# Performance work log

Measured on AMD Instinct MI355X. Metric: run time of the kernel, lower is better.

The kernel has to match this reference:

```python
import jax, jax.numpy as jnp
import numpy as np


def setup_inputs() -> dict:
    key = jax.random.key(0)
    k1, k2, k3, k4, k5 = jax.random.split(key, 5)
    B, L, H = 32, 2048, 768
    in1 = jax.random.normal(k1, (B, H), dtype=jnp.float32)
    in2 = jax.random.normal(k2, (B, H), dtype=jnp.float32)
    text = jax.random.normal(k3, (B, L, H), dtype=jnp.float32)
    textmask = jnp.ones((B, L), dtype=jnp.float32)  # 1 = valid token
    # learned params (nn.Linear weights are [out, in]); small scale avoids tanh saturation
    W2 = jax.random.normal(k4, (H, 3 * H), dtype=jnp.float32) * 0.02
    b2 = jnp.zeros((H,), dtype=jnp.float32)
    W1 = jax.random.normal(k5, (1, H), dtype=jnp.float32) * 0.02
    b1 = jnp.zeros((1,), dtype=jnp.float32)
    return {"in1": in1, "in2": in2, "text": text, "textmask": textmask,
            "W2": W2, "b2": b2, "W1": W1, "b1": b1}


def reference(in1, in2, text, textmask, W2, b2, W1, b1):
    H = in1.shape[-1]
    # Split linear2 weight along input dim instead of materializing cat([in1,in2,text]).
    # Same math: cat @ W2.T == in1@W2a.T + in2@W2b.T + text@W2c.T
    W2a, W2b, W2c = W2[:, :H], W2[:, H:2 * H], W2[:, 2 * H:]
    bias_bh = in1 @ W2a.T + in2 @ W2b.T + b2          # [B, H], broadcast over L
    h = jnp.tanh(jnp.einsum('blh,gh->blg', text, W2c) + bias_bh[:, None, :])  # [B, L, H]
    att = jnp.einsum('blh,h->bl', h, W1[0]) + b1[0]   # [B, L]
    att = jax.nn.softmax((1.0 - textmask) * (-1e20) + att, axis=-1)  # masked softmax [B, L]
    context = jnp.einsum('bl,blh->bh', att, text)     # weighted sum [B, H]
    return context, att[:, None, :]                   # matches (context, att[B,1,L])
```

## Files before the change

kernel.cpp:

```cpp
#include <hip/hip_runtime.h>
#include <hip/hip_bf16.h>

typedef __bf16 bf16x8 __attribute__((ext_vector_type(8)));
typedef __bf16 bf16x4 __attribute__((ext_vector_type(4)));
typedef float  f32x4  __attribute__((ext_vector_type(4)));

#define H 768
#define LSEQ 2048
#define BATCH 32
#define MROWS (BATCH*LSEQ)
#define NT 3
#define W2S 2304

__device__ __forceinline__ void gload_lds16(const void* g, void* l){
  __builtin_amdgcn_global_load_lds((const __attribute__((address_space(1))) void*)g,
                                   (__attribute__((address_space(3))) void*)l, 16, 0, 0);
}

__global__ void w2c_cvt_k(const float* __restrict__ W2, __bf16* __restrict__ w2cb){
  int i4 = blockIdx.x*256 + threadIdx.x;
  int g  = i4 / 192;
  int hc = (i4 % 192) * 4;
  f32x4 v = *(const f32x4*)(W2 + (size_t)g*W2S + 1536 + hc);
  bf16x4 o; o[0]=(__bf16)v[0]; o[1]=(__bf16)v[1]; o[2]=(__bf16)v[2]; o[3]=(__bf16)v[3];
  *(bf16x4*)(w2cb + (size_t)g*H + hc) = o;
}

__global__ void bias_k(const float* __restrict__ in1, const float* __restrict__ in2,
                       const float* __restrict__ W2, const float* __restrict__ b2,
                       float* __restrict__ bias){
  int b = blockIdx.y;
  int g = blockIdx.x*64 + (threadIdx.x & 63);
  int q = threadIdx.x >> 6;
  const float* wa = W2 + (size_t)g*W2S + q*192;
  const float* wb = wa + H;
  const float* x1 = in1 + b*H + q*192;
  const float* x2 = in2 + b*H + q*192;
  float acc = 0.f;
  #pragma unroll 8
  for (int h=0; h<192; h+=4){
    f32x4 a4 = *(const f32x4*)(wa+h);
    f32x4 c4 = *(const f32x4*)(x1+h);
    f32x4 b4 = *(const f32x4*)(wb+h);
    f32x4 d4 = *(const f32x4*)(x2+h);
    acc += a4[0]*c4[0]+a4[1]*c4[1]+a4[2]*c4[2]+a4[3]*c4[3];
    acc += b4[0]*d4[0]+b4[1]*d4[1]+b4[2]*d4[2]+b4[3]*d4[3];
  }
  __shared__ float sm[4][64];
  sm[q][threadIdx.x&63] = acc;
  __syncthreads();
  if (q==0){
    float r = sm[0][threadIdx.x]+sm[1][threadIdx.x]+sm[2][threadIdx.x]+sm[3][threadIdx.x] + b2[g];
    bias[(size_t)b*H + g] = r;
  }
}

__global__ __launch_bounds__(256,2) void fused_gemm_att_k(
    const float* __restrict__ text, const __bf16* __restrict__ w2cb,
    const float* __restrict__ bias, const float* __restrict__ W1,
    float* __restrict__ attp)
{
  __shared__ __align__(16) __bf16 a_lds[2][128*32];
  __shared__ __align__(16) __bf16 b_lds[2][256*32];
  __shared__ float att_lds[2][128];

  int bid = blockIdx.x;
  int lin = (bid & 7)*192 + (bid >> 3);
  int mt  = lin / 3;
  int nt  = lin % 3;
  int b   = mt >> 4;
  int m0  = mt << 7;
  int t = threadIdx.x, lane = t & 63, wid = t >> 6;
  int wm = wid >> 1, wn = wid & 1;

  const float*  atile = text + (size_t)m0*H;
  const __bf16* btile = w2cb + (size_t)(nt*256)*H;

  f32x4 acc[4][8];
  #pragma unroll
  for (int mi=0;mi<4;++mi)
    #pragma unroll
    for (int ni=0;ni<8;++ni) acc[mi][ni] = (f32x4){0.f,0.f,0.f,0.f};

  int ar = t>>3, ac = (t&7)*4;
  int ag = (t&7)>>1, ah = t&1;
  f32x4 aReg[4];

  auto loadA = [&](int kk){
    #pragma unroll
    for (int j=0;j<4;++j)
      aReg[j] = *(const f32x4*)(atile + (size_t)(ar + j*32)*H + kk*32 + ac);
  };
  auto writeA = [&](int bf){
    #pragma unroll
    for (int j=0;j<4;++j){
      int row = ar + j*32;
      int gc  = ag ^ ((row>>1)&3);
      bf16x4 o; o[0]=(__bf16)aReg[j][0]; o[1]=(__bf16)aReg[j][1];
                o[2]=(__bf16)aReg[j][2]; o[3]=(__bf16)aReg[j][3];
      *(bf16x4*)&a_lds[bf][row*32 + gc*8 + ah*4] = o;
    }
  };
  auto stageB = [&](int bf, int kk){
    #pragma unroll
    for (int j=0;j<4;++j){
      int slot = wid*4 + j;
      int n  = slot*16 + (lane>>2);
      int gs = (lane&3) ^ ((lane>>3)&3);
      gload_lds16(btile + (size_t)n*H + kk*32 + gs*8, &b_lds[bf][slot*512]);
    }
  };
  auto compute = [&](int bf){
    bf16x8 af[4];
    #pragma unroll
    for (int mi=0;mi<4;++mi){
      int row = wm*64 + mi*16 + (lane&15);
      int rc  = (lane>>4) ^ ((row>>1)&3);
      af[mi] = *(const bf16x8*)&a_lds[bf][row*32 + rc*8];
    }
    #pragma unroll
    for (int ni=0;ni<8;++ni){
      int n  = wn*128 + ni*16 + (lane&15);
      int rc = (lane>>4) ^ ((n>>1)&3);
      bf16x8 bq = *(const bf16x8*)&b_lds[bf][n*32 + rc*8];
      #pragma unroll
      for (int mi=0;mi<4;++mi)
        acc[mi][ni] = __builtin_amdgcn_mfma_f32_16x16x32_bf16(af[mi], bq, acc[mi][ni], 0,0,0);
    }
  };

  loadA(0);
  writeA(0);
  stageB(0, 0);
  loadA(1);
  __syncthreads();

  #pragma unroll 2
  for (int kk=0; kk<22; ++kk){
    int cur = kk&1, nxt = cur^1;
    stageB(nxt, kk+1);
    writeA(nxt);
    loadA(kk+2);
    compute(cur);
    asm volatile("s_waitcnt vmcnt(4) lgkmcnt(0)" ::: "memory");
    __builtin_amdgcn_sched_barrier(0);
    __builtin_amdgcn_s_barrier();
    __builtin_amdgcn_sched_barrier(0);
  }
  {
    stageB(1, 23);
    writeA(1);
    compute(0);
    asm volatile("s_waitcnt vmcnt(0) lgkmcnt(0)" ::: "memory");
    __builtin_amdgcn_sched_barrier(0);
    __builtin_amdgcn_s_barrier();
    __builtin_amdgcn_sched_barrier(0);
  }
  compute(1);

  float bb[8], ww[8];
  int gb = nt*256 + wn*128 + (lane&15);
  #pragma unroll
  for (int ni=0;ni<8;++ni){ bb[ni]=bias[(size_t)b*H + gb + ni*16]; ww[ni]=W1[gb + ni*16]; }

  float av[16];
  #pragma unroll
  for (int mi=0;mi<4;++mi)
    #pragma unroll
    for (int r=0;r<4;++r){
      float s = 0.f;
      #pragma unroll
      for (int ni=0;ni<8;++ni){
        float x = acc[mi][ni][r] + bb[ni];
        float e = __expf(2.0f*x);
        s += ww[ni] * ((e-1.0f)*__builtin_amdgcn_rcpf(e+1.0f));
      }
      av[mi*4+r] = s;
    }
  #pragma unroll
  for (int off=1; off<16; off<<=1)
    #pragma unroll
    for (int i=0;i<16;++i) av[i] += __shfl_xor(av[i], off);

  if ((lane&15)==0){
    int mg = (lane>>4)*4;
    #pragma unroll
    for (int mi=0;mi<4;++mi)
      #pragma unroll
      for (int r=0;r<4;++r)
        att_lds[wn][wm*64 + mi*16 + mg + r] = av[mi*4+r];
  }
  __syncthreads();
  if (t < 128) attp[(size_t)nt*MROWS + m0 + t] = att_lds[0][t] + att_lds[1][t];
}

__global__ void softmax_k(const float* __restrict__ attp, const float* __restrict__ tmask,
                          const float* __restrict__ b1, float* __restrict__ att){
  int b = blockIdx.x, t = threadIdx.x;
  int lane = t & 63, wv = t >> 6;
  __shared__ float sl[LSEQ];
  __shared__ float red[4];
  float b1v = b1[0];
  float lmax = -3.0e38f;
  for (int i=t; i<LSEQ; i+=256){
    float v = b1v;
    #pragma unroll
    for (int p=0;p<NT;++p) v += attp[(size_t)p*MROWS + b*LSEQ + i];
    v += (1.0f - tmask[b*LSEQ+i]) * -1.0e20f;
    sl[i] = v;
    lmax = fmaxf(lmax, v);
  }
  #pragma unroll
  for (int off=32; off>=1; off>>=1) lmax = fmaxf(lmax, __shfl_xor(lmax, off));
  if (lane==0) red[wv] = lmax;
  __syncthreads();
  float mx = fmaxf(fmaxf(red[0],red[1]), fmaxf(red[2],red[3]));
  __syncthreads();
  float lsum = 0.f;
  for (int i=t; i<LSEQ; i+=256){
    float e = __expf(sl[i]-mx);
    sl[i] = e;
    lsum += e;
  }
  #pragma unroll
  for (int off=32; off>=1; off>>=1) lsum += __shfl_xor(lsum, off);
  if (lane==0) red[wv] = lsum;
  __syncthreads();
  float inv = 1.0f/(red[0]+red[1]+red[2]+red[3]);
  for (int i=t; i<LSEQ; i+=256) att[(size_t)b*LSEQ+i] = sl[i]*inv;
}

__global__ void ctxpart_k(const float* __restrict__ text, const float* __restrict__ att,
                          float* __restrict__ ctxp){
  int chunk = blockIdx.x, b = blockIdx.y, t = threadIdx.x;
  const float* tp = text + ((size_t)(b*LSEQ + chunk*64))*H + 4*t;
  const float* ap = att + (size_t)b*LSEQ + chunk*64;
  f32x4 acc = {0.f,0.f,0.f,0.f};
  #pragma unroll 4
  for (int l=0;l<64;++l){
    float a = ap[l];
    f32x4 v = *(const f32x4*)(tp + (size_t)l*H);
    acc[0] += a*v[0]; acc[1] += a*v[1]; acc[2] += a*v[2]; acc[3] += a*v[3];
  }
  *(f32x4*)(ctxp + ((size_t)(b*32+chunk))*H + 4*t) = acc;
}

__global__ void ctxred_k(const float* __restrict__ ctxp, float* __restrict__ out){
  int b = blockIdx.x, h = threadIdx.x;
  float s = 0.f;
  #pragma unroll 8
  for (int c=0;c<32;++c) s += ctxp[((size_t)(b*32+c))*H + h];
  out[(size_t)b*H + h] = s;
}

extern "C" void kernel_launch(void* const* d_in, const int* in_sizes, int n_in,
                              void* d_out, int out_size, void* d_ws, size_t ws_size,
                              hipStream_t stream){
  (void)in_sizes; (void)n_in; (void)out_size; (void)ws_size;
  const float* in1   = (const float*)d_in[0];
  const float* in2   = (const float*)d_in[1];
  const float* text  = (const float*)d_in[2];
  const float* tmask = (const float*)d_in[3];
  const float* W2    = (const float*)d_in[4];
  const float* b2    = (const float*)d_in[5];
  const float* W1    = (const float*)d_in[6];
  const float* b1    = (const float*)d_in[7];
  float* out = (float*)d_out;
  char*  ws  = (char*)d_ws;
  __bf16* w2cb = (__bf16*)(ws);
  float* biasb = (float*)(ws + 1179648);
  float* attp  = (float*)(ws + 1277952);
  float* ctxp  = (float*)(ws + 2850816);
  float* att_out = out + BATCH*H;

  w2c_cvt_k      <<<dim3(576),   dim3(256), 0, stream>>>(W2, w2cb);
  bias_k         <<<dim3(12,32), dim3(256), 0, stream>>>(in1, in2, W2, b2, biasb);
  fused_gemm_att_k<<<dim3(1536), dim3(256), 0, stream>>>(text, w2cb, biasb, W1, attp);
  softmax_k      <<<dim3(32),    dim3(256), 0, stream>>>(attp, tmask, b1, att_out);
  ctxpart_k      <<<dim3(32,32), dim3(192), 0, stream>>>(text, att_out, ctxp);
  ctxred_k       <<<dim3(32),    dim3(768), 0, stream>>>(ctxp, out);
}
```

Before: 182.0 us.

## Retile fused GEMM to 128x128 output tiles with 64-wide K steps

Shrinks each block's N tile from 256 to 128 columns and doubles the K step from 32 to 64, doubling the grid and producing six partial attention sums instead of three. The A-tile load becomes contiguous per thread with wider 16-byte LDS writes, and the XOR swizzles are precomputed. The aim is fewer accumulator registers, better latency hiding and fewer loop iterations and barriers. The cost is that each fp32 text tile is read and converted to bf16 twice as often, and the extra reads must be absorbed by L2.

```diff
diff --git a/kernel.cpp b/kernel.cpp
--- a/kernel.cpp
+++ b/kernel.cpp
@@ -9,7 +9,7 @@
 #define LSEQ 2048
 #define BATCH 32
 #define MROWS (BATCH*LSEQ)
-#define NT 3
+#define NT 6
 #define W2S 2304
 
 __device__ __forceinline__ void gload_lds16(const void* g, void* l){
@@ -60,72 +60,91 @@
     const float* __restrict__ bias, const float* __restrict__ W1,
     float* __restrict__ attp)
 {
-  __shared__ __align__(16) __bf16 a_lds[2][128*32];
-  __shared__ __align__(16) __bf16 b_lds[2][256*32];
+  __shared__ __align__(16) __bf16 a_lds[2][128*64];
+  __shared__ __align__(16) __bf16 b_lds[2][128*64];
   __shared__ float att_lds[2][128];
 
   int bid = blockIdx.x;
-  int lin = (bid & 7)*192 + (bid >> 3);
-  int mt  = lin / 3;
-  int nt  = lin % 3;
-  int b   = mt >> 4;
+  int lin = (bid & 7)*384 + (bid >> 3);
+  int mt  = lin / 6;
+  int nt  = lin % 6;
   int m0  = mt << 7;
+  int b   = m0 >> 11;
   int t = threadIdx.x, lane = t & 63, wid = t >> 6;
   int wm = wid >> 1, wn = wid & 1;
+  int fr = lane & 15, fc = lane >> 4;
 
   const float*  atile = text + (size_t)m0*H;
-  const __bf16* btile = w2cb + (size_t)(nt*256)*H;
-
-  f32x4 acc[4][8];
+  const __bf16* btile = w2cb + (size_t)(nt*128)*H;
+
+  f32x4 acc[4][4];
   #pragma unroll
   for (int mi=0;mi<4;++mi)
     #pragma unroll
-    for (int ni=0;ni<8;++ni) acc[mi][ni] = (f32x4){0.f,0.f,0.f,0.f};
-
-  int ar = t>>3, ac = (t&7)*4;
-  int ag = (t&7)>>1, ah = t&1;
-  f32x4 aReg[4];
+    for (int ni=0;ni<4;++ni) acc[mi][ni] = (f32x4){0.f,0.f,0.f,0.f};
+
+  int arow = t>>1, ahalf = t&1;
+  const float* aptr = atile + (size_t)arow*H + ahalf*32;
+  int awOff[4];
+  #pragma unroll
+  for (int j=0;j<4;++j) awOff[j] = arow*64 + ((ahalf*4 + j) ^ (arow&7))*8;
+  f32x4 aReg[8];
+
+  const __bf16* bsrc[4];
+  int bdst[4];
+  #pragma unroll
+  for (int jj=0;jj<4;++jj){
+    int slot = wid*4 + jj;
+    int n = slot*8 + (lane>>3);
+    bsrc[jj] = btile + (size_t)n*H + ((lane&7)^(n&7))*8;
+    bdst[jj] = slot*512 + lane*8;
+  }
+
+  int offA[2][4], offB[2][4];
+  #pragma unroll
+  for (int h=0;h<2;++h)
+    #pragma unroll
+    for (int i=0;i<4;++i){
+      int row = wm*64 + i*16 + fr;
+      offA[h][i] = row*64 + (((h<<2)|fc) ^ (row&7))*8;
+      int n = wn*64 + i*16 + fr;
+      offB[h][i] = n*64 + (((h<<2)|fc) ^ (n&7))*8;
+    }
 
   auto loadA = [&](int kk){
     #pragma unroll
-    for (int j=0;j<4;++j)
-      aReg[j] = *(const f32x4*)(atile + (size_t)(ar + j*32)*H + kk*32 + ac);
+    for (int j=0;j<8;++j) aReg[j] = *(const f32x4*)(aptr + kk*64 + j*4);
   };
   auto writeA = [&](int bf){
     #pragma unroll
     for (int j=0;j<4;++j){
-      int row = ar + j*32;
-      int gc  = ag ^ ((row>>1)&3);
-      bf16x4 o; o[0]=(__bf16)aReg[j][0]; o[1]=(__bf16)aReg[j][1];
-                o[2]=(__bf16)aReg[j][2]; o[3]=(__bf16)aReg[j][3];
-      *(bf16x4*)&a_lds[bf][row*32 + gc*8 + ah*4] = o;
+      bf16x8 v;
+      v[0]=(__bf16)aReg[2*j][0]; v[1]=(__bf16)aReg[2*j][1];
+      v[2]=(__bf16)aReg[2*j][2]; v[3]=(__bf16)aReg[2*j][3];
+      v[4]=(__bf16)aReg[2*j+1][0]; v[5]=(__bf16)aReg[2*j+1][1];
+      v[6]=(__bf16)aReg[2*j+1][2]; v[7]=(__bf16)aReg[2*j+1][3];
+      *(bf16x8*)&a_lds[bf][awOff[j]] = v;
     }
   };
   auto stageB = [&](int bf, int kk){
     #pragma unroll
-    for (int j=0;j<4;++j){
-      int slot = wid*4 + j;
-      int n  = slot*16 + (lane>>2);
-      int gs = (lane&3) ^ ((lane>>3)&3);
-      gload_lds16(btile + (size_t)n*H + kk*32 + gs*8, &b_lds[bf][slot*512]);
-    }
+    for (int jj=0;jj<4;++jj)
+      gload_lds16(bsrc[jj] + kk*64, &b_lds[bf][bdst[jj]]);
   };
   auto compute = [&](int bf){
-    bf16x8 af[4];
-    #pragma unroll
-    for (int mi=0;mi<4;++mi){
-      int row = wm*64 + mi*16 + (lane&15);
-      int rc  = (lane>>4) ^ ((row>>1)&3);
-      af[mi] = *(const bf16x8*)&a_lds[bf][row*32 + rc*8];
-    }
-    #pragma unroll
-    for (int ni=0;ni<8;++ni){
-      int n  = wn*128 + ni*16 + (lane&15);
-      int rc = (lane>>4) ^ ((n>>1)&3);
-      bf16x8 bq = *(const bf16x8*)&b_lds[bf][n*32 + rc*8];
+    #pragma unroll
+    for (int h=0;h<2;++h){
+      bf16x8 af[4], bq[4];
+      #pragma unroll
+      for (int i=0;i<4;++i){
+        af[i] = *(const bf16x8*)&a_lds[bf][offA[h][i]];
+        bq[i] = *(const bf16x8*)&b_lds[bf][offB[h][i]];
+      }
       #pragma unroll
       for (int mi=0;mi<4;++mi)
-        acc[mi][ni] = __builtin_amdgcn_mfma_f32_16x16x32_bf16(af[mi], bq, acc[mi][ni], 0,0,0);
+        #pragma unroll
+        for (int ni=0;ni<4;++ni)
+          acc[mi][ni] = __builtin_amdgcn_mfma_f32_16x16x32_bf16(af[mi], bq[ni], acc[mi][ni], 0,0,0);
     }
   };
 
@@ -133,22 +152,23 @@
   writeA(0);
   stageB(0, 0);
   loadA(1);
-  __syncthreads();
+  asm volatile("s_waitcnt vmcnt(0) lgkmcnt(0)" ::: "memory");
+  __builtin_amdgcn_s_barrier();
 
   #pragma unroll 2
-  for (int kk=0; kk<22; ++kk){
+  for (int kk=0; kk<10; ++kk){
     int cur = kk&1, nxt = cur^1;
     stageB(nxt, kk+1);
     writeA(nxt);
     loadA(kk+2);
     compute(cur);
-    asm volatile("s_waitcnt vmcnt(4) lgkmcnt(0)" ::: "memory");
+    asm volatile("s_waitcnt vmcnt(8) lgkmcnt(0)" ::: "memory");
     __builtin_amdgcn_sched_barrier(0);
     __builtin_amdgcn_s_barrier();
     __builtin_amdgcn_sched_barrier(0);
   }
   {
-    stageB(1, 23);
+    stageB(1, 11);
     writeA(1);
     compute(0);
     asm volatile("s_waitcnt vmcnt(0) lgkmcnt(0)" ::: "memory");
@@ -158,10 +178,10 @@
   }
   compute(1);
 
-  float bb[8], ww[8];
-  int gb = nt*256 + wn*128 + (lane&15);
-  #pragma unroll
-  for (int ni=0;ni<8;++ni){ bb[ni]=bias[(size_t)b*H + gb + ni*16]; ww[ni]=W1[gb + ni*16]; }
+  float bb[4], ww[4];
+  int gb = nt*128 + wn*64 + fr;
+  #pragma unroll
+  for (int ni=0;ni<4;++ni){ bb[ni]=bias[(size_t)b*H + gb + ni*16]; ww[ni]=W1[gb + ni*16]; }
 
   float av[16];
   #pragma unroll
@@ -170,7 +190,7 @@
     for (int r=0;r<4;++r){
       float s = 0.f;
       #pragma unroll
-      for (int ni=0;ni<8;++ni){
+      for (int ni=0;ni<4;++ni){
         float x = acc[mi][ni][r] + bb[ni];
         float e = __expf(2.0f*x);
         s += ww[ni] * ((e-1.0f)*__builtin_amdgcn_rcpf(e+1.0f));
@@ -182,13 +202,12 @@
     #pragma unroll
     for (int i=0;i<16;++i) av[i] += __shfl_xor(av[i], off);
 
-  if ((lane&15)==0){
-    int mg = (lane>>4)*4;
+  if (fr==0){
     #pragma unroll
     for (int mi=0;mi<4;++mi)
       #pragma unroll
       for (int r=0;r<4;++r)
-        att_lds[wn][wm*64 + mi*16 + mg + r] = av[mi*4+r];
+        att_lds[wn][wm*64 + mi*16 + fc*4 + r] = av[mi*4+r];
   }
   __syncthreads();
   if (t < 128) attp[(size_t)nt*MROWS + m0 + t] = att_lds[0][t] + att_lds[1][t];
@@ -275,7 +294,7 @@
 
   w2c_cvt_k      <<<dim3(576),   dim3(256), 0, stream>>>(W2, w2cb);
   bias_k         <<<dim3(12,32), dim3(256), 0, stream>>>(in1, in2, W2, b2, biasb);
-  fused_gemm_att_k<<<dim3(1536), dim3(256), 0, stream>>>(text, w2cb, biasb, W1, attp);
+  fused_gemm_att_k<<<dim3(3072), dim3(256), 0, stream>>>(text, w2cb, biasb, W1, attp);
   softmax_k      <<<dim3(32),    dim3(256), 0, stream>>>(attp, tmask, b1, att_out);
   ctxpart_k      <<<dim3(32,32), dim3(192), 0, stream>>>(text, att_out, ctxp);
   ctxred_k       <<<dim3(32),    dim3(768), 0, stream>>>(ctxp, out);
```

Result: slower. 262.3 us (+44.1%).
